# Kernel optimization log

Hardware: AMD Instinct MI355X
Metric: run time of the kernel (lower is better)

## Reference

```python
import jax, jax.numpy as jnp
import numpy as np

D_MODEL = 1024
N_HEADS = 16
D_K = D_MODEL // N_HEADS
D_HIDDEN = 2048
LN_EPS = 1e-5


def setup_inputs() -> dict:
    key = jax.random.key(0)
    ks = jax.random.split(key, 16)
    s = 0.02
    inp = {
        'x': jax.random.normal(ks[0], (4, 2048, D_MODEL), dtype=jnp.float32),
        'Wq': jax.random.normal(ks[1], (D_MODEL, D_MODEL), dtype=jnp.float32) * s,
        'bq': jnp.zeros((D_MODEL,), jnp.float32),
        'Wk': jax.random.normal(ks[2], (D_MODEL, D_MODEL), dtype=jnp.float32) * s,
        'bk': jnp.zeros((D_MODEL,), jnp.float32),
        'Wv': jax.random.normal(ks[3], (D_MODEL, D_MODEL), dtype=jnp.float32) * s,
        'bv': jnp.zeros((D_MODEL,), jnp.float32),
        'Wo': jax.random.normal(ks[4], (D_MODEL, D_MODEL), dtype=jnp.float32) * s,
        'bo': jnp.zeros((D_MODEL,), jnp.float32),
        'ln1_g': jnp.ones((D_MODEL,), jnp.float32),
        'ln1_b': jnp.zeros((D_MODEL,), jnp.float32),
        'ln2_g': jnp.ones((D_MODEL,), jnp.float32),
        'ln2_b': jnp.zeros((D_MODEL,), jnp.float32),
        'W1': jax.random.normal(ks[5], (2 * D_HIDDEN, D_MODEL), dtype=jnp.float32) * s,
        'b1': jnp.zeros((2 * D_HIDDEN,), jnp.float32),
        'W2': jax.random.normal(ks[6], (D_MODEL, D_HIDDEN), dtype=jnp.float32) * s,
        'b2': jnp.zeros((D_MODEL,), jnp.float32),
    }
    return inp


def _layernorm(x, g, b):
    mu = jnp.mean(x, axis=-1, keepdims=True)
    var = jnp.mean(jnp.square(x - mu), axis=-1, keepdims=True)
    return (x - mu) * jax.lax.rsqrt(var + LN_EPS) * g + b


def _attention(xn, Wq, bq, Wk, bk, Wv, bv, Wo, bo):
    B, S, _ = xn.shape
    def split_heads(t):  # [B,S,D] -> [B,H,S,Dk]
        return t.reshape(B, S, N_HEADS, D_K).transpose(0, 2, 1, 3)
    Q = split_heads(xn @ Wq.T + bq)
    K = split_heads(xn @ Wk.T + bk)
    V = split_heads(xn @ Wv.T + bv)
    scores = jnp.einsum('bhqd,bhkd->bhqk', Q, K) / jnp.float32(D_K ** 0.5)
    attn = jax.nn.softmax(scores, axis=-1)  # torch code does max-sub + softmax (same math)
    ctx = jnp.einsum('bhqk,bhkd->bhqd', attn, V)
    ctx = ctx.transpose(0, 2, 1, 3).reshape(B, S, D_MODEL)
    return ctx @ Wo.T + bo


def reference(x, Wq, bq, Wk, bk, Wv, bv, Wo, bo, ln1_g, ln1_b, ln2_g, ln2_b, W1, b1, W2, b2):
    # pre-norm attention block
    xn = _layernorm(x, ln1_g, ln1_b)
    x = x + _attention(xn, Wq, bq, Wk, bk, Wv, bv, Wo, bo)
    # pre-norm ReGLU FFN
    xn = _layernorm(x, ln2_g, ln2_b)
    h = xn @ W1.T + b1
    a, b_ = jnp.split(h, 2, axis=-1)
    h = jax.nn.relu(a) * b_
    x = x + (h @ W2.T + b2)
    return x
```

## Files before the change

### kernel.cpp

```cpp
#include <hip/hip_runtime.h>
#include <hip/hip_bf16.h>

typedef __attribute__((ext_vector_type(8))) short short8;
typedef __attribute__((ext_vector_type(4))) float floatx4;

#define LN_EPS 1e-5f
#define EXP2_SCALE 0.18033688011112042f

__device__ __forceinline__ float b2f(unsigned short u) {
    union { float f; unsigned int i; } x; x.i = ((unsigned int)u) << 16; return x.f;
}
__device__ __forceinline__ unsigned short f2b(float f) {
    union { float f; unsigned int i; } x; x.f = f;
    unsigned int r = x.i + 0x7fffu + ((x.i >> 16) & 1u);
    return (unsigned short)(r >> 16);
}
__device__ __forceinline__ unsigned int cvtpk(float a, float b) {
    unsigned int r;
    asm("v_cvt_pk_bf16_f32 %0, %1, %2" : "=v"(r) : "v"(a), "v"(b));
    return r;
}

__device__ __forceinline__ void async16(const unsigned short* g, unsigned short* l) {
    __builtin_amdgcn_global_load_lds(
        (const __attribute__((address_space(1))) unsigned int*)g,
        (__attribute__((address_space(3))) unsigned int*)l, 16, 0, 0);
}

template<typename T>
__device__ __forceinline__ void ln_row(const T* __restrict__ xr, const float* __restrict__ g,
                                       const float* __restrict__ bb, unsigned short* __restrict__ outr,
                                       float* red)
{
    const int tid = threadIdx.x;
    float v[4];
    if constexpr (sizeof(T) == 4) {
        float4 t = *reinterpret_cast<const float4*>(xr + tid * 4);
        v[0] = t.x; v[1] = t.y; v[2] = t.z; v[3] = t.w;
    } else {
        ushort4 t = *reinterpret_cast<const ushort4*>(xr + tid * 4);
        v[0] = b2f(t.x); v[1] = b2f(t.y); v[2] = b2f(t.z); v[3] = b2f(t.w);
    }
    float s  = v[0] + v[1] + v[2] + v[3];
    float sq = v[0]*v[0] + v[1]*v[1] + v[2]*v[2] + v[3]*v[3];
#pragma unroll
    for (int o = 32; o >= 1; o >>= 1) {
        s  += __shfl_xor(s,  o, 64);
        sq += __shfl_xor(sq, o, 64);
    }
    const int wave = tid >> 6, lane = tid & 63;
    if (lane == 0) { red[wave] = s; red[4 + wave] = sq; }
    __syncthreads();
    s  = red[0] + red[1] + red[2] + red[3];
    sq = red[4] + red[5] + red[6] + red[7];
    const float mu  = s * (1.0f / 1024.0f);
    const float var = sq * (1.0f / 1024.0f) - mu * mu;
    const float rs  = rsqrtf(var + LN_EPS);
    float4 g4 = *reinterpret_cast<const float4*>(g  + tid * 4);
    float4 b4 = *reinterpret_cast<const float4*>(bb + tid * 4);
    float r0 = (v[0] - mu) * rs * g4.x + b4.x;
    float r1 = (v[1] - mu) * rs * g4.y + b4.y;
    float r2 = (v[2] - mu) * rs * g4.z + b4.z;
    float r3 = (v[3] - mu) * rs * g4.w + b4.w;
    *reinterpret_cast<uint2*>(outr + tid * 4) = make_uint2(cvtpk(r0, r1), cvtpk(r2, r3));
}

__global__ __launch_bounds__(256)
void prep_kernel(const float* __restrict__ Wq, const float* __restrict__ Wk,
                 const float* __restrict__ Wv, const float* __restrict__ Wo,
                 const float* __restrict__ W1, const float* __restrict__ W2,
                 unsigned short* __restrict__ wdst,
                 const float* __restrict__ x, const float* __restrict__ ln1g,
                 const float* __restrict__ ln1b, unsigned short* __restrict__ xn)
{
    __shared__ float red[8];
    if (blockIdx.x < 5120) {
        const size_t i = (size_t)(blockIdx.x * 256 + threadIdx.x) * 8;
        const float* src; size_t off;
        if (i < 4194304) {
            int w = (int)(i >> 20);
            src = (w == 0) ? Wq : (w == 1) ? Wk : (w == 2) ? Wv : Wo;
            off = i & 1048575;
        } else if (i < 8388608) { src = W1; off = i - 4194304; }
        else                    { src = W2; off = i - 8388608; }
        float4 a = *reinterpret_cast<const float4*>(src + off);
        float4 b = *reinterpret_cast<const float4*>(src + off + 4);
        short8 r;
        r[0] = (short)f2b(a.x); r[1] = (short)f2b(a.y);
        r[2] = (short)f2b(a.z); r[3] = (short)f2b(a.w);
        r[4] = (short)f2b(b.x); r[5] = (short)f2b(b.y);
        r[6] = (short)f2b(b.z); r[7] = (short)f2b(b.w);
        *reinterpret_cast<short8*>(wdst + i) = r;
    } else {
        const int row = blockIdx.x - 5120;
        ln_row<float>(x + (size_t)row * 1024, ln1g, ln1b, xn + (size_t)row * 1024, red);
    }
}

__global__ __launch_bounds__(256)
void ln_kernel(const unsigned short* __restrict__ x, const float* __restrict__ g,
               const float* __restrict__ bb, unsigned short* __restrict__ out)
{
    __shared__ float red[8];
    const int row = blockIdx.x;
    ln_row<unsigned short>(x + (size_t)row * 1024, g, bb, out + (size_t)row * 1024, red);
}

template<int EPI>
__global__ __launch_bounds__(256, 3)
void gemm_nt(const unsigned short* __restrict__ A, const unsigned short* __restrict__ B,
             const float* __restrict__ bias, const void* __restrict__ res,
             void* __restrict__ C, int M, int N, int K)
{
    __shared__ unsigned short As[128 * 64];
    __shared__ unsigned short Bs[128 * 64];
    const int m0 = blockIdx.y * 128, n0 = blockIdx.x * 128;
    const int tid = threadIdx.x, wave = tid >> 6, lane = tid & 63;
    const int wm = (wave >> 1) * 64, wn = (wave & 1) * 64;
    const int lrow = lane & 15, quad = lane >> 4;
    const int srow = wave * 32 + (lane >> 3);
    const int scol = (((lane & 7) ^ ((lane >> 3) & 7)) << 3);
    const int ca0 = (quad ^ (lrow & 7)) << 3;
    const int ca1 = ((quad + 4) ^ (lrow & 7)) << 3;

    floatx4 acc[4][4] = {};
    const unsigned short* gA = A + (size_t)(m0 + srow) * K + scol;
    const unsigned short* gB = B + (size_t)(n0 + srow) * K + scol;
    unsigned short* lA = &As[(wave * 32) * 64];
    unsigned short* lB = &Bs[(wave * 32) * 64];

    for (int k0 = 0; k0 < K; k0 += 64) {
        __syncthreads();
#pragma unroll
        for (int r = 0; r < 4; r++) {
            async16(gA + k0 + (size_t)(r * 8) * K, lA + r * 8 * 64);
            async16(gB + k0 + (size_t)(r * 8) * K, lB + r * 8 * 64);
        }
        __syncthreads();
#pragma unroll
        for (int ks = 0; ks < 2; ks++) {
            const int ca = ks ? ca1 : ca0;
            short8 af[4], bf[4];
#pragma unroll
            for (int i = 0; i < 4; i++)
                af[i] = *reinterpret_cast<const short8*>(&As[(wm + i * 16 + lrow) * 64 + ca]);
#pragma unroll
            for (int j = 0; j < 4; j++)
                bf[j] = *reinterpret_cast<const short8*>(&Bs[(wn + j * 16 + lrow) * 64 + ca]);
#pragma unroll
            for (int i = 0; i < 4; i++)
#pragma unroll
                for (int j = 0; j < 4; j++)
                    acc[i][j] = __builtin_amdgcn_mfma_f32_16x16x32_bf16(af[i], bf[j], acc[i][j], 0, 0, 0);
        }
    }

#pragma unroll
    for (int i = 0; i < 4; i++) {
        int rb = m0 + wm + i * 16 + quad * 4;
#pragma unroll
        for (int j = 0; j < 4; j++) {
            int col = n0 + wn + j * 16 + lrow;
            float bv = bias[col];
#pragma unroll
            for (int r = 0; r < 4; r++) {
                size_t idx = (size_t)(rb + r) * N + col;
                float v = acc[i][j][r] + bv;
                if (EPI == 1) {
                    v += ((const float*)res)[idx];
                    ((unsigned short*)C)[idx] = f2b(v);
                } else {
                    v += b2f(((const unsigned short*)res)[idx]);
                    ((float*)C)[idx] = v;
                }
            }
        }
    }
}

__global__ __launch_bounds__(256, 3)
void gemm_qkv(const unsigned short* __restrict__ A, const unsigned short* __restrict__ Wqkv,
              const float* __restrict__ bq, const float* __restrict__ bk, const float* __restrict__ bv,
              unsigned short* __restrict__ QK, unsigned short* __restrict__ Vt)
{
    __shared__ unsigned short As[128 * 64];
    __shared__ unsigned short Bs[128 * 64];
    const int part = blockIdx.x >> 3;
    const int m0 = blockIdx.y * 128, n0 = (blockIdx.x & 7) * 128;
    const int tid = threadIdx.x, wave = tid >> 6, lane = tid & 63;
    const int wm = (wave >> 1) * 64, wn = (wave & 1) * 64;
    const int lrow = lane & 15, quad = lane >> 4;
    const int srow = wave * 32 + (lane >> 3);
    const int scol = (((lane & 7) ^ ((lane >> 3) & 7)) << 3);
    const int ca0 = (quad ^ (lrow & 7)) << 3;
    const int ca1 = ((quad + 4) ^ (lrow & 7)) << 3;
    const unsigned short* B = Wqkv + (size_t)part * 1048576;
    const float* bias = (part == 0) ? bq : (part == 1) ? bk : bv;

    floatx4 acc[4][4] = {};
    const unsigned short* gA = A + (size_t)(m0 + srow) * 1024 + scol;
    const unsigned short* gB = B + (size_t)(n0 + srow) * 1024 + scol;
    unsigned short* lA = &As[(wave * 32) * 64];
    unsigned short* lB = &Bs[(wave * 32) * 64];

    for (int k0 = 0; k0 < 1024; k0 += 64) {
        __syncthreads();
#pragma unroll
        for (int r = 0; r < 4; r++) {
            async16(gA + k0 + (size_t)(r * 8) * 1024, lA + r * 8 * 64);
            async16(gB + k0 + (size_t)(r * 8) * 1024, lB + r * 8 * 64);
        }
        __syncthreads();
#pragma unroll
        for (int ks = 0; ks < 2; ks++) {
            const int ca = ks ? ca1 : ca0;
            short8 af[4], bf[4];
#pragma unroll
            for (int i = 0; i < 4; i++)
                af[i] = *reinterpret_cast<const short8*>(&As[(wm + i * 16 + lrow) * 64 + ca]);
#pragma unroll
            for (int j = 0; j < 4; j++)
                bf[j] = *reinterpret_cast<const short8*>(&Bs[(wn + j * 16 + lrow) * 64 + ca]);
#pragma unroll
            for (int i = 0; i < 4; i++)
#pragma unroll
                for (int j = 0; j < 4; j++)
                    acc[i][j] = __builtin_amdgcn_mfma_f32_16x16x32_bf16(af[i], bf[j], acc[i][j], 0, 0, 0);
        }
    }

#pragma unroll
    for (int i = 0; i < 4; i++) {
        int rb = m0 + wm + i * 16 + quad * 4;
#pragma unroll
        for (int j = 0; j < 4; j++) {
            int col = n0 + wn + j * 16 + lrow;
            float bv2 = bias[col];
            if (part == 0) {
#pragma unroll
                for (int r = 0; r < 4; r++)
                    QK[(size_t)(rb + r) * 1024 + col] = f2b((acc[i][j][r] + bv2) * EXP2_SCALE);
            } else if (part == 1) {
                unsigned short* dst = QK + 8388608;
#pragma unroll
                for (int r = 0; r < 4; r++)
                    dst[(size_t)(rb + r) * 1024 + col] = f2b(acc[i][j][r] + bv2);
            } else {
                int b = rb >> 11, spos = rb & 2047;
                int h = col >> 6, d = col & 63;
                unsigned short* dst = Vt + (((size_t)(b * 16 + h) * 64 + d) << 11) + spos;
                unsigned int u01 = cvtpk(acc[i][j][0] + bv2, acc[i][j][1] + bv2);
                unsigned int u23 = cvtpk(acc[i][j][2] + bv2, acc[i][j][3] + bv2);
                *reinterpret_cast<uint2*>(dst) = make_uint2(u01, u23);
            }
        }
    }
}

__global__ __launch_bounds__(256, 2)
void gemm_w1_reglu(const unsigned short* __restrict__ A, const unsigned short* __restrict__ B,
                   const float* __restrict__ bias, unsigned short* __restrict__ G)
{
    __shared__ unsigned short As[128 * 64];
    __shared__ unsigned short B0s[128 * 64];
    __shared__ unsigned short B1s[128 * 64];
    const int m0 = blockIdx.y * 128, n0 = blockIdx.x * 128;
    const int tid = threadIdx.x, wave = tid >> 6, lane = tid & 63;
    const int wm = (wave >> 1) * 64, wn = (wave & 1) * 64;
    const int lrow = lane & 15, quad = lane >> 4;
    const int srow = wave * 32 + (lane >> 3);
    const int scol = (((lane & 7) ^ ((lane >> 3) & 7)) << 3);
    const int ca0 = (quad ^ (lrow & 7)) << 3;
    const int ca1 = ((quad + 4) ^ (lrow & 7)) << 3;

    floatx4 acca[4][4] = {};
    floatx4 accb[4][4] = {};
    const unsigned short* gA  = A + (size_t)(m0 + srow) * 1024 + scol;
    const unsigned short* gB0 = B + (size_t)(n0 + srow) * 1024 + scol;
    const unsigned short* gB1 = B + (size_t)(2048 + n0 + srow) * 1024 + scol;
    unsigned short* lA  = &As [(wave * 32) * 64];
    unsigned short* lB0 = &B0s[(wave * 32) * 64];
    unsigned short* lB1 = &B1s[(wave * 32) * 64];

    for (int k0 = 0; k0 < 1024; k0 += 64) {
        __syncthreads();
#pragma unroll
        for (int r = 0; r < 4; r++) {
            async16(gA  + k0 + (size_t)(r * 8) * 1024, lA  + r * 8 * 64);
            async16(gB0 + k0 + (size_t)(r * 8) * 1024, lB0 + r * 8 * 64);
            async16(gB1 + k0 + (size_t)(r * 8) * 1024, lB1 + r * 8 * 64);
        }
        __syncthreads();
#pragma unroll
        for (int ks = 0; ks < 2; ks++) {
            const int ca = ks ? ca1 : ca0;
            short8 af[4], b0[4], b1[4];
#pragma unroll
            for (int i = 0; i < 4; i++)
                af[i] = *reinterpret_cast<const short8*>(&As[(wm + i * 16 + lrow) * 64 + ca]);
#pragma unroll
            for (int j = 0; j < 4; j++) {
                b0[j] = *reinterpret_cast<const short8*>(&B0s[(wn + j * 16 + lrow) * 64 + ca]);
                b1[j] = *reinterpret_cast<const short8*>(&B1s[(wn + j * 16 + lrow) * 64 + ca]);
            }
#pragma unroll
            for (int i = 0; i < 4; i++)
#pragma unroll
                for (int j = 0; j < 4; j++) {
                    acca[i][j] = __builtin_amdgcn_mfma_f32_16x16x32_bf16(af[i], b0[j], acca[i][j], 0, 0, 0);
                    accb[i][j] = __builtin_amdgcn_mfma_f32_16x16x32_bf16(af[i], b1[j], accb[i][j], 0, 0, 0);
                }
        }
    }

#pragma unroll
    for (int i = 0; i < 4; i++) {
        int rb = m0 + wm + i * 16 + quad * 4;
#pragma unroll
        for (int j = 0; j < 4; j++) {
            int col = n0 + wn + j * 16 + lrow;
            float ba = bias[col], bb2 = bias[2048 + col];
#pragma unroll
            for (int r = 0; r < 4; r++) {
                float va = acca[i][j][r] + ba;
                float vb = accb[i][j][r] + bb2;
                G[(size_t)(rb + r) * 2048 + col] = f2b(fmaxf(va, 0.0f) * vb);
            }
        }
    }
}

__global__ __launch_bounds__(256, 4)
void attn_kernel(const unsigned short* __restrict__ Qm, const unsigned short* __restrict__ Km,
                 const unsigned short* __restrict__ Vt, unsigned short* __restrict__ ctx)
{
    __shared__ unsigned short Ks[64 * 64];
    __shared__ unsigned short Vs[64 * 64];
    __shared__ unsigned short Ps[4][32][72];

    const int tid = threadIdx.x, wave = tid >> 6, lane = tid & 63;
    const int lrow = lane & 15, quad = lane >> 4;
    const int id = blockIdx.x + (blockIdx.y << 4);
    const int qb = id >> 6;
    const int bh = ((id & 7) << 3) + ((id >> 3) & 7);
    const size_t base  = (size_t)(bh >> 4) * 2048 * 1024 + (size_t)(bh & 15) * 64;
    const size_t vbase = (size_t)bh * 131072;
    const int q0 = qb * 128 + wave * 32;
    const int g_sub = (lane >> 3);
    const int g_col = (((lane & 7) ^ (g_sub & 7)) << 3);
    const int ca0 = (quad ^ (lrow & 7)) << 3;
    const int ca1 = ((quad + 4) ^ (lrow & 7)) << 3;

    short8 qf[2][2];
#pragma unroll
    for (int m = 0; m < 2; m++) {
        const unsigned short* qp = Qm + base + (size_t)(q0 + m * 16 + lrow) * 1024 + quad * 8;
        qf[m][0] = *reinterpret_cast<const short8*>(qp);
        qf[m][1] = *reinterpret_cast<const short8*>(qp + 32);
    }

    floatx4 o[2][4] = {};
    float li[2] = {0.f, 0.f};
    const floatx4 fzero = {0.f, 0.f, 0.f, 0.f};

    for (int t = 0; t < 32; t++) {
        const int k0 = t * 64;
        __syncthreads();
#pragma unroll
        for (int r = 0; r < 2; r++) {
            int krow = wave * 16 + r * 8 + g_sub;
            async16(Km + base + (size_t)(k0 + krow) * 1024 + g_col, &Ks[(wave * 16 + r * 8) * 64]);
            async16(Vt + vbase + (size_t)krow * 2048 + k0 + g_col,  &Vs[(wave * 16 + r * 8) * 64]);
        }
        __syncthreads();

        short8 kf0[4], kf1[4];
#pragma unroll
        for (int j = 0; j < 4; j++) {
            kf0[j] = *reinterpret_cast<const short8*>(&Ks[(j * 16 + lrow) * 64 + ca0]);
            kf1[j] = *reinterpret_cast<const short8*>(&Ks[(j * 16 + lrow) * 64 + ca1]);
        }
        floatx4 s4t[2][4];
        __builtin_amdgcn_s_setprio(1);
#pragma unroll
        for (int m = 0; m < 2; m++)
#pragma unroll
            for (int j = 0; j < 4; j++) {
                s4t[m][j] = __builtin_amdgcn_mfma_f32_16x16x32_bf16(kf0[j], qf[m][0], fzero, 0, 0, 0);
                s4t[m][j] = __builtin_amdgcn_mfma_f32_16x16x32_bf16(kf1[j], qf[m][1], s4t[m][j], 0, 0, 0);
            }
        __builtin_amdgcn_s_setprio(0);

#pragma unroll
        for (int m = 0; m < 2; m++) {
            float acc = 0.f;
#pragma unroll
            for (int j = 0; j < 4; j++) {
                float p0 = __builtin_amdgcn_exp2f(s4t[m][j][0]);
                float p1 = __builtin_amdgcn_exp2f(s4t[m][j][1]);
                float p2 = __builtin_amdgcn_exp2f(s4t[m][j][2]);
                float p3 = __builtin_amdgcn_exp2f(s4t[m][j][3]);
                acc += (p0 + p1) + (p2 + p3);
                uint2 pk = make_uint2(cvtpk(p0, p1), cvtpk(p2, p3));
                *reinterpret_cast<uint2*>(&Ps[wave][m * 16 + lrow][j * 16 + quad * 4]) = pk;
            }
            li[m] += acc;
        }
        __asm__ volatile("s_waitcnt lgkmcnt(0)" ::: "memory");

        short8 pf[2][2];
#pragma unroll
        for (int m = 0; m < 2; m++) {
            pf[m][0] = *reinterpret_cast<const short8*>(&Ps[wave][m * 16 + lrow][quad * 8]);
            pf[m][1] = *reinterpret_cast<const short8*>(&Ps[wave][m * 16 + lrow][32 + quad * 8]);
        }
#pragma unroll
        for (int jj = 0; jj < 4; jj++) {
            short8 vf0 = *reinterpret_cast<const short8*>(&Vs[(jj * 16 + lrow) * 64 + ca0]);
            short8 vf1 = *reinterpret_cast<const short8*>(&Vs[(jj * 16 + lrow) * 64 + ca1]);
            __builtin_amdgcn_s_setprio(1);
#pragma unroll
            for (int m = 0; m < 2; m++) {
                o[m][jj] = __builtin_amdgcn_mfma_f32_16x16x32_bf16(pf[m][0], vf0, o[m][jj], 0, 0, 0);
                o[m][jj] = __builtin_amdgcn_mfma_f32_16x16x32_bf16(pf[m][1], vf1, o[m][jj], 0, 0, 0);
            }
            __builtin_amdgcn_s_setprio(0);
        }
    }

#pragma unroll
    for (int m = 0; m < 2; m++) {
        float l = li[m];
        l += __shfl_xor(l, 16, 64);
        l += __shfl_xor(l, 32, 64);
        float inv = 1.0f / l;
#pragma unroll
        for (int r = 0; r < 4; r++) {
            float invr = __shfl(inv, quad * 4 + r, 64);
            int srow = q0 + m * 16 + quad * 4 + r;
#pragma unroll
            for (int jj = 0; jj < 4; jj++)
                ctx[base + (size_t)srow * 1024 + jj * 16 + lrow] = f2b(o[m][jj][r] * invr);
        }
    }
}

extern "C" void kernel_launch(void* const* d_in, const int* in_sizes, int n_in,
                              void* d_out, int out_size, void* d_ws, size_t ws_size,
                              hipStream_t stream) {
    const float* x    = (const float*)d_in[0];
    const float* Wq   = (const float*)d_in[1];
    const float* bq   = (const float*)d_in[2];
    const float* Wk   = (const float*)d_in[3];
    const float* bk   = (const float*)d_in[4];
    const float* Wv   = (const float*)d_in[5];
    const float* bv   = (const float*)d_in[6];
    const float* Wo   = (const float*)d_in[7];
    const float* bo   = (const float*)d_in[8];
    const float* ln1g = (const float*)d_in[9];
    const float* ln1b = (const float*)d_in[10];
    const float* ln2g = (const float*)d_in[11];
    const float* ln2b = (const float*)d_in[12];
    const float* W1   = (const float*)d_in[13];
    const float* b1   = (const float*)d_in[14];
    const float* W2   = (const float*)d_in[15];
    const float* b2   = (const float*)d_in[16];
    float* out = (float*)d_out;

    char* ws = (char*)d_ws;
    unsigned short* wflat = (unsigned short*)ws;
    unsigned short* wqb = wflat;
    unsigned short* wob = wflat + 3145728;
    unsigned short* w1b = wflat + 4194304;
    unsigned short* w2b = wflat + 8388608;
    unsigned short* xn  = (unsigned short*)(ws + 20971520);
    unsigned short* Qm  = (unsigned short*)(ws + 37748736);
    unsigned short* x1b = (unsigned short*)(ws + 37748736);
    unsigned short* Vt  = (unsigned short*)(ws + 71303168);
    unsigned short* g   = (unsigned short*)(ws + 71303168);

    dim3 blk(256);
    prep_kernel<<<13312, blk, 0, stream>>>(Wq, Wk, Wv, Wo, W1, W2, wflat, x, ln1g, ln1b, xn);
    gemm_qkv<<<dim3(24, 64), blk, 0, stream>>>(xn, wqb, bq, bk, bv, Qm, Vt);
    attn_kernel<<<dim3(16, 64), blk, 0, stream>>>(Qm, Qm + 8388608, Vt, xn);
    gemm_nt<1><<<dim3(8, 64), blk, 0, stream>>>(xn, wob, bo, x, x1b, 8192, 1024, 1024);
    ln_kernel<<<8192, blk, 0, stream>>>(x1b, ln2g, ln2b, xn);
    gemm_w1_reglu<<<dim3(16, 64), blk, 0, stream>>>(xn, w1b, b1, g);
    gemm_nt<2><<<dim3(8, 64), blk, 0, stream>>>(g, w2b, b2, x1b, out, 8192, 1024, 2048);
}
```

Measured before the change: 432.3 us.

## Double-buffer attention K/V tiles and keep P in registers via permuted V layout

The attention kernel now double-buffers the K and V shared-memory tiles, issuing async loads for the next tile before computing the current one, with explicit vmcnt waits and barriers. The softmax probabilities are packed directly into MFMA operand registers instead of round-tripping through a per-wave LDS buffer. This works because the QKV GEMM now writes V transposed with a permuted sequence order inside each 32-position group. The QKV kernel's occupancy hint is also raised from 3 to 4. The change trades extra LDS for the second buffer and relies on the permutation exactly matching the MFMA register layout.

```diff
diff --git a/kernel.cpp b/kernel.cpp
--- a/kernel.cpp
+++ b/kernel.cpp
@@ -178,7 +178,7 @@
     }
 }
 
-__global__ __launch_bounds__(256, 3)
+__global__ __launch_bounds__(256, 4)
 void gemm_qkv(const unsigned short* __restrict__ A, const unsigned short* __restrict__ Wqkv,
               const float* __restrict__ bq, const float* __restrict__ bk, const float* __restrict__ bv,
               unsigned short* __restrict__ QK, unsigned short* __restrict__ Vt)
@@ -247,8 +247,10 @@
                     dst[(size_t)(rb + r) * 1024 + col] = f2b(acc[i][j][r] + bv2);
             } else {
                 int b = rb >> 11, spos = rb & 2047;
+                int local = spos & 31;
+                int sposP = (spos & ~31) | (((local >> 2) & 3) * 8 + ((local >> 4) << 2));
                 int h = col >> 6, d = col & 63;
-                unsigned short* dst = Vt + (((size_t)(b * 16 + h) * 64 + d) << 11) + spos;
+                unsigned short* dst = Vt + (((size_t)(b * 16 + h) * 64 + d) << 11) + sposP;
                 unsigned int u01 = cvtpk(acc[i][j][0] + bv2, acc[i][j][1] + bv2);
                 unsigned int u23 = cvtpk(acc[i][j][2] + bv2, acc[i][j][3] + bv2);
                 *reinterpret_cast<uint2*>(dst) = make_uint2(u01, u23);
@@ -334,9 +336,8 @@
 void attn_kernel(const unsigned short* __restrict__ Qm, const unsigned short* __restrict__ Km,
                  const unsigned short* __restrict__ Vt, unsigned short* __restrict__ ctx)
 {
-    __shared__ unsigned short Ks[64 * 64];
-    __shared__ unsigned short Vs[64 * 64];
-    __shared__ unsigned short Ps[4][32][72];
+    __shared__ unsigned short Ks[2][64 * 64];
+    __shared__ unsigned short Vs[2][64 * 64];
 
     const int tid = threadIdx.x, wave = tid >> 6, lane = tid & 63;
     const int lrow = lane & 15, quad = lane >> 4;
@@ -358,27 +359,27 @@
         qf[m][0] = *reinterpret_cast<const short8*>(qp);
         qf[m][1] = *reinterpret_cast<const short8*>(qp + 32);
     }
+    __asm__ volatile("s_waitcnt vmcnt(0)" ::: "memory");
 
     floatx4 o[2][4] = {};
     float li[2] = {0.f, 0.f};
     const floatx4 fzero = {0.f, 0.f, 0.f, 0.f};
 
-    for (int t = 0; t < 32; t++) {
-        const int k0 = t * 64;
-        __syncthreads();
+    auto stage = [&](int buf, int k0) {
 #pragma unroll
         for (int r = 0; r < 2; r++) {
             int krow = wave * 16 + r * 8 + g_sub;
-            async16(Km + base + (size_t)(k0 + krow) * 1024 + g_col, &Ks[(wave * 16 + r * 8) * 64]);
-            async16(Vt + vbase + (size_t)krow * 2048 + k0 + g_col,  &Vs[(wave * 16 + r * 8) * 64]);
-        }
-        __syncthreads();
-
+            async16(Km + base + (size_t)(k0 + krow) * 1024 + g_col, &Ks[buf][(wave * 16 + r * 8) * 64]);
+            async16(Vt + vbase + (size_t)krow * 2048 + k0 + g_col,  &Vs[buf][(wave * 16 + r * 8) * 64]);
+        }
+    };
+
+    auto compute = [&](int buf) {
         short8 kf0[4], kf1[4];
 #pragma unroll
         for (int j = 0; j < 4; j++) {
-            kf0[j] = *reinterpret_cast<const short8*>(&Ks[(j * 16 + lrow) * 64 + ca0]);
-            kf1[j] = *reinterpret_cast<const short8*>(&Ks[(j * 16 + lrow) * 64 + ca1]);
+            kf0[j] = *reinterpret_cast<const short8*>(&Ks[buf][(j * 16 + lrow) * 64 + ca0]);
+            kf1[j] = *reinterpret_cast<const short8*>(&Ks[buf][(j * 16 + lrow) * 64 + ca1]);
         }
         floatx4 s4t[2][4];
         __builtin_amdgcn_s_setprio(1);
@@ -391,9 +392,11 @@
             }
         __builtin_amdgcn_s_setprio(0);
 
+        short8 pfs[2][2];
 #pragma unroll
         for (int m = 0; m < 2; m++) {
             float acc = 0.f;
+            unsigned int dw[8];
 #pragma unroll
             for (int j = 0; j < 4; j++) {
                 float p0 = __builtin_amdgcn_exp2f(s4t[m][j][0]);
@@ -401,32 +404,42 @@
                 float p2 = __builtin_amdgcn_exp2f(s4t[m][j][2]);
                 float p3 = __builtin_amdgcn_exp2f(s4t[m][j][3]);
                 acc += (p0 + p1) + (p2 + p3);
-                uint2 pk = make_uint2(cvtpk(p0, p1), cvtpk(p2, p3));
-                *reinterpret_cast<uint2*>(&Ps[wave][m * 16 + lrow][j * 16 + quad * 4]) = pk;
+                dw[2 * j]     = cvtpk(p0, p1);
+                dw[2 * j + 1] = cvtpk(p2, p3);
             }
             li[m] += acc;
-        }
-        __asm__ volatile("s_waitcnt lgkmcnt(0)" ::: "memory");
-
-        short8 pf[2][2];
-#pragma unroll
-        for (int m = 0; m < 2; m++) {
-            pf[m][0] = *reinterpret_cast<const short8*>(&Ps[wave][m * 16 + lrow][quad * 8]);
-            pf[m][1] = *reinterpret_cast<const short8*>(&Ps[wave][m * 16 + lrow][32 + quad * 8]);
-        }
+            pfs[m][0] = *reinterpret_cast<const short8*>(&dw[0]);
+            pfs[m][1] = *reinterpret_cast<const short8*>(&dw[4]);
+        }
+
 #pragma unroll
         for (int jj = 0; jj < 4; jj++) {
-            short8 vf0 = *reinterpret_cast<const short8*>(&Vs[(jj * 16 + lrow) * 64 + ca0]);
-            short8 vf1 = *reinterpret_cast<const short8*>(&Vs[(jj * 16 + lrow) * 64 + ca1]);
+            short8 vf0 = *reinterpret_cast<const short8*>(&Vs[buf][(jj * 16 + lrow) * 64 + ca0]);
+            short8 vf1 = *reinterpret_cast<const short8*>(&Vs[buf][(jj * 16 + lrow) * 64 + ca1]);
             __builtin_amdgcn_s_setprio(1);
 #pragma unroll
             for (int m = 0; m < 2; m++) {
-                o[m][jj] = __builtin_amdgcn_mfma_f32_16x16x32_bf16(pf[m][0], vf0, o[m][jj], 0, 0, 0);
-                o[m][jj] = __builtin_amdgcn_mfma_f32_16x16x32_bf16(pf[m][1], vf1, o[m][jj], 0, 0, 0);
+                o[m][jj] = __builtin_amdgcn_mfma_f32_16x16x32_bf16(pfs[m][0], vf0, o[m][jj], 0, 0, 0);
+                o[m][jj] = __builtin_amdgcn_mfma_f32_16x16x32_bf16(pfs[m][1], vf1, o[m][jj], 0, 0, 0);
             }
             __builtin_amdgcn_s_setprio(0);
         }
-    }
+    };
+
+    stage(0, 0);
+    for (int t = 0; t < 31; t++) {
+        stage((t + 1) & 1, (t + 1) << 6);
+        __asm__ volatile("s_waitcnt vmcnt(4)" ::: "memory");
+        __builtin_amdgcn_s_barrier();
+        __builtin_amdgcn_sched_barrier(0);
+        compute(t & 1);
+        __builtin_amdgcn_sched_barrier(0);
+        __builtin_amdgcn_s_barrier();
+    }
+    __asm__ volatile("s_waitcnt vmcnt(0)" ::: "memory");
+    __builtin_amdgcn_s_barrier();
+    __builtin_amdgcn_sched_barrier(0);
+    compute(1);
 
 #pragma unroll
     for (int m = 0; m < 2; m++) {
```

After: 422.6 us. 2.2% less time.
